# Optimization experiments

Hardware: AMD Instinct MI355X
Metric: run time of the kernel (lower is better)

Reference implementation:

```python
import jax, jax.numpy as jnp
import numpy as np

B, S, D, H = 2, 2048, 1024, 16
HD = D // H  # head_dim = 64
ROPE_BASE = 10000.0
INIT_STD = 0.02


def setup_inputs() -> dict:
    key = jax.random.key(0)
    k1, k2, k3 = jax.random.split(key, 3)
    x = jax.random.normal(k1, (B, S, D), dtype=jnp.float32)
    w_qkv = jax.random.normal(k2, (3 * D, D), dtype=jnp.float32) * INIT_STD
    w_out = jax.random.normal(k3, (D, D), dtype=jnp.float32) * (1.0 / np.sqrt(D))
    b_out = jnp.zeros((D,), dtype=jnp.float32)
    return {"x": x, "w_qkv": w_qkv, "w_out": w_out, "b_out": b_out}


def _rope_cos_sin(s_len, head_dim, dtype):
    theta = 1.0 / ROPE_BASE ** (jnp.arange(0, head_dim, 2, dtype=jnp.float32) / head_dim)
    freqs = jnp.outer(jnp.arange(s_len, dtype=jnp.float32), theta)  # [s, d/2]
    freqs = jnp.concatenate([freqs, freqs], axis=-1)  # [s, d]
    return jnp.cos(freqs).astype(dtype), jnp.sin(freqs).astype(dtype)


def _apply_rope(qk, cos, sin):
    # qk: [b, h, s, d]; rotate-half: (-x2, x1)
    d2 = qk.shape[-1] // 2
    x1, x2 = qk[..., :d2], qk[..., d2:]
    rot = jnp.concatenate([-x2, x1], axis=-1)
    return qk * cos + rot * sin


def reference(x, w_qkv, w_out, b_out):
    b, s, d = x.shape
    qkv = jnp.einsum('bsd,ed->bse', x, w_qkv)  # [b, s, 3D]
    qkv = qkv.reshape(b, s, 3 * H, HD).transpose(0, 2, 1, 3)  # [b, 3h, s, d]
    qk, v = qkv[:, :2 * H], qkv[:, 2 * H:]
    cos, sin = _rope_cos_sin(s, HD, x.dtype)
    qk = _apply_rope(qk, cos, sin)
    q, k = qk[:, :H], qk[:, H:]
    scale = 1.0 / np.sqrt(HD)
    scores = jnp.einsum('bhqd,bhkd->bhqk', q, k) * scale  # [b, h, s, s]
    causal = jnp.tril(jnp.ones((s, s), dtype=bool))
    scores = jnp.where(causal, scores, jnp.finfo(scores.dtype).min)
    attn = jax.nn.softmax(scores, axis=-1)
    o = jnp.einsum('bhqk,bhkd->bhqd', attn, v)  # [b, h, s, d]
    o = o.transpose(0, 2, 1, 3).reshape(b, s, d)
    return jnp.einsum('bsd,ed->bse', o, w_out) + b_out
```

## Files before the change

### kernel.cpp

```cpp
#include <hip/hip_runtime.h>
#include <hip/hip_fp16.h>
#include <math.h>

#define B_  2
#define S_  2048
#define D_  1024
#define H_  16
#define HD_ 64

typedef _Float16  f16;
typedef __attribute__((ext_vector_type(8))) _Float16 f16x8;
typedef __attribute__((ext_vector_type(4))) _Float16 f16x4;
typedef __attribute__((ext_vector_type(4))) float    f32x4;

#define LOG2E 1.4426950408889634f
#define L2_10000_DIV32 0.41524101186092029f
#define PS 72

__device__ __forceinline__ float fin(float v) { return (v == v) ? v : 0.0f; }

__device__ __forceinline__ f16x8 cvt8(const float* p) {
  float4 a = *(const float4*)p;
  float4 b = *(const float4*)(p + 4);
  f16x8 h;
  h[0] = (f16)a.x; h[1] = (f16)a.y; h[2] = (f16)a.z; h[3] = (f16)a.w;
  h[4] = (f16)b.x; h[5] = (f16)b.y; h[6] = (f16)b.z; h[7] = (f16)b.w;
  return h;
}

__device__ __forceinline__ void gload16(const f16* g, f16* l) {
  __builtin_amdgcn_global_load_lds(
      (__attribute__((address_space(1))) void*)(const_cast<f16*>(g)),
      (__attribute__((address_space(3))) void*)l, 16, 0, 0);
}

__global__ void __launch_bounds__(256)
k_cvt3(const float* __restrict__ wq, const float* __restrict__ wo,
       const float* __restrict__ x,
       f16* __restrict__ wqh, f16* __restrict__ woh, f16* __restrict__ xh,
       int doX)
{
  const int NWQ = 3 * D_ * D_ / 4, NWO = D_ * D_ / 4, NX = B_ * S_ * D_ / 4;
  const int n = NWQ + NWO + (doX ? NX : 0);
  for (int i = blockIdx.x * 256 + threadIdx.x; i < n; i += gridDim.x * 256) {
    const float* src; f16* dst; int j;
    if (i < NWQ)            { src = wq; dst = wqh; j = i; }
    else if (i < NWQ + NWO) { src = wo; dst = woh; j = i - NWQ; }
    else                    { src = x;  dst = xh;  j = i - NWQ - NWO; }
    float4 v = ((const float4*)src)[j];
    f16x4 h = {(f16)v.x, (f16)v.y, (f16)v.z, (f16)v.w};
    ((f16x4*)dst)[j] = h;
  }
}

template <bool XF16>
__global__ void __launch_bounds__(256)
k_qkv_rope(const float* __restrict__ xf, const f16* __restrict__ xh,
           const f16* __restrict__ wqh,
           f16* __restrict__ Qb, f16* __restrict__ Kb, f16* __restrict__ Vt)
{
  __shared__ __align__(16) f16 As[128 * 64];
  __shared__ __align__(16) f16 Bs[128 * 64];
  const int t = threadIdx.x;
  const int w = t >> 6;
  const int lane = t & 63;
  const int ll = lane & 15;
  const int quad = lane >> 4;
  const int wm = w >> 1, wn = w & 1;
  const int row0 = blockIdx.y * 128;
  const int col0 = blockIdx.x * 128;

  const f32x4 fz = {0.f, 0.f, 0.f, 0.f};
  f32x4 acc[4][4];
#pragma unroll
  for (int i = 0; i < 4; ++i)
#pragma unroll
    for (int j = 0; j < 4; ++j) acc[i][j] = fz;

  const int ldr = t >> 3;
  const int ldk = (t & 7) * 8;
  const float* gaf = xf  + (size_t)(row0 + ldr) * D_ + ldk;
  const f16*   gah = xh  + (size_t)(row0 + ldr) * D_ + ldk;
  const f16*   gb  = wqh + (size_t)(col0 + ldr) * D_ + ldk;

  for (int kt = 0; kt < D_; kt += 64) {
#pragma unroll
    for (int i = 0; i < 4; ++i) {
      gload16(gb + (size_t)i * 32 * D_ + kt, &Bs[(i * 32 + w * 8) * 64]);
      if (XF16) gload16(gah + (size_t)i * 32 * D_ + kt, &As[(i * 32 + w * 8) * 64]);
    }
    if (!XF16) {
      f16x8 ra[4];
#pragma unroll
      for (int i = 0; i < 4; ++i) ra[i] = cvt8(gaf + (size_t)i * 32 * D_ + kt);
#pragma unroll
      for (int i = 0; i < 4; ++i)
        *(f16x8*)&As[(i * 32 + ldr) * 64 + ldk] = ra[i];
    }
    __syncthreads();
#pragma unroll
    for (int kk = 0; kk < 64; kk += 32) {
      f16x8 a[4], b[4];
#pragma unroll
      for (int mt = 0; mt < 4; ++mt)
        a[mt] = *(const f16x8*)&As[(wm * 64 + mt * 16 + ll) * 64 + kk + quad * 8];
#pragma unroll
      for (int nt = 0; nt < 4; ++nt)
        b[nt] = *(const f16x8*)&Bs[(wn * 64 + nt * 16 + ll) * 64 + kk + quad * 8];
#pragma unroll
      for (int mt = 0; mt < 4; ++mt)
#pragma unroll
        for (int nt = 0; nt < 4; ++nt)
          acc[mt][nt] = __builtin_amdgcn_mfma_f32_16x16x32_f16(
              a[mt], b[nt], acc[mt][nt], 0, 0, 0);
    }
    __syncthreads();
  }

  const int h3 = (col0 >> 6) + wn;
  if (h3 < 32) {
    f16* dst = (h3 < 16) ? Qb : Kb;
    const int h = (h3 < 16) ? h3 : h3 - 16;
    const float th0 = exp2f(-(float)ll * L2_10000_DIV32);
    const float th1 = exp2f(-(float)(16 + ll) * L2_10000_DIV32);
#pragma unroll
    for (int mt = 0; mt < 4; ++mt) {
#pragma unroll
      for (int r = 0; r < 4; ++r) {
        const int row = row0 + wm * 64 + mt * 16 + quad * 4 + r;
        const int b = row >> 11;
        const int p = row & (S_ - 1);
        f16* base = dst + ((size_t)(b * H_ + h) * S_ + p) * HD_;
        const float fp = (float)p;
        float s0, c0, s1, c1;
        sincosf(fp * th0, &s0, &c0);
        sincosf(fp * th1, &s1, &c1);
        {
          float x1 = acc[mt][0][r], x2 = acc[mt][2][r];
          base[ll]      = (f16)fin(x1 * c0 - x2 * s0);
          base[ll + 32] = (f16)fin(x2 * c0 + x1 * s0);
        }
        {
          float x1 = acc[mt][1][r], x2 = acc[mt][3][r];
          base[16 + ll]      = (f16)fin(x1 * c1 - x2 * s1);
          base[16 + ll + 32] = (f16)fin(x2 * c1 + x1 * s1);
        }
      }
    }
  } else {
    const int hv = h3 - 32;
#pragma unroll
    for (int mt = 0; mt < 4; ++mt)
#pragma unroll
      for (int nt = 0; nt < 4; ++nt)
#pragma unroll
        for (int r = 0; r < 4; ++r) {
          const int row = row0 + wm * 64 + mt * 16 + quad * 4 + r;
          const int b = row >> 11;
          const int p = row & (S_ - 1);
          const int dd = nt * 16 + ll;
          Vt[((size_t)(b * H_ + hv) * HD_ + dd) * S_ + p] = (f16)fin(acc[mt][nt][r]);
        }
  }
}

__device__ __forceinline__ void softmax_tile(
    f32x4 sc[4], bool diag, int qloc, int ll, int quad,
    float& mrun, float& lrun, float& alpha, f16* Pt)
{
  float pm = -3.0e4f;
#pragma unroll
  for (int nt = 0; nt < 4; ++nt)
#pragma unroll
    for (int r = 0; r < 4; ++r) {
      float s = sc[nt][r];
      s = (s == s) ? s : -3.0e4f;
      if (diag && (nt * 16 + quad * 4 + r) > qloc) s = -3.0e4f;
      sc[nt][r] = s;
      pm = fmaxf(pm, s);
    }
  pm = fmaxf(pm, __shfl_xor(pm, 16));
  pm = fmaxf(pm, __shfl_xor(pm, 32));
  const float mn = fmaxf(mrun, pm);
  alpha = exp2f(mrun - mn);
  mrun = mn;
  float ps = 0.f;
#pragma unroll
  for (int nt = 0; nt < 4; ++nt) {
    f16x4 pk;
#pragma unroll
    for (int r = 0; r < 4; ++r) {
      float p = exp2f(sc[nt][r] - mn);
      ps += p;
      pk[r] = (f16)p;
    }
    *(f16x4*)&Pt[ll * PS + nt * 16 + quad * 4] = pk;
  }
  ps += __shfl_xor(ps, 16);
  ps += __shfl_xor(ps, 32);
  lrun = lrun * alpha + ps;
}

__device__ __forceinline__ void write_o(
    f32x4 acco[4], float lrun, f16* Pt, int ll, int quad, int w,
    int qt, size_t bh, f16* Ob)
{
  const float inv = 1.0f / fmaxf(lrun, 1e-30f);
#pragma unroll
  for (int dg = 0; dg < 4; ++dg) {
    f16x4 ov;
#pragma unroll
    for (int r = 0; r < 4; ++r) ov[r] = (f16)fin(acco[dg][r] * inv);
    *(f16x4*)&Pt[ll * PS + dg * 16 + quad * 4] = ov;
  }
#pragma unroll
  for (int s2 = 0; s2 < 2; ++s2) {
    f16x8 o = *(const f16x8*)&Pt[ll * PS + (quad + 4 * s2) * 8];
    const size_t row = bh * S_ + qt * 64 + w * 16 + ll;
    *(f16x8*)&Ob[row * HD_ + (quad + 4 * s2) * 8] = o;
  }
}

__global__ void __launch_bounds__(256, 2)
k_attn2(const f16* Qb, const f16* __restrict__ Kb,
        const f16* __restrict__ Vt, f16* Ob)
{
  __shared__ __align__(16) f16 Qs[128 * PS];
  __shared__ __align__(16) f16 Ks[2][64 * PS];
  __shared__ __align__(16) f16 Vs[2][64 * PS];
  __shared__ __align__(16) f16 Ps[4][16 * PS];

  const int t = threadIdx.x;
  const int w = t >> 6;
  const int lane = t & 63;
  const int ll = lane & 15;
  const int quad = lane >> 4;
  const int qtA = blockIdx.x;
  const int qtB = 31 - qtA;
  const int h = blockIdx.y;
  const int b = blockIdx.z;
  const size_t bh = (size_t)b * H_ + h;
  const f16* Qg = Qb + bh * S_ * HD_;
  const f16* Kg = Kb + bh * S_ * HD_;
  const f16* Vg = Vt + bh * HD_ * S_;

  {
    const int r = t >> 1;
    const int c0 = (t & 1) * 32;
    const int grow = (r < 64) ? (qtA * 64 + r) : (qtB * 64 + r - 64);
    const f16 hsc = (f16)(0.125f * LOG2E);
#pragma unroll
    for (int j = 0; j < 4; ++j) {
      f16x8 v = *(const f16x8*)(Qg + (size_t)grow * HD_ + c0 + j * 8);
#pragma unroll
      for (int e = 0; e < 8; ++e) v[e] *= hsc;
      *(f16x8*)&Qs[r * PS + c0 + j * 8] = v;
    }
  }
  {
    const int r = t >> 2;
    const int c = (t & 3) * 16;
    f16x8 a0 = *(const f16x8*)(Kg + (size_t)r * HD_ + c);
    f16x8 a1 = *(const f16x8*)(Kg + (size_t)r * HD_ + c + 8);
    f16x8 b0 = *(const f16x8*)(Vg + (size_t)r * S_ + c);
    f16x8 b1 = *(const f16x8*)(Vg + (size_t)r * S_ + c + 8);
    *(f16x8*)&Ks[0][r * PS + c]     = a0;
    *(f16x8*)&Ks[0][r * PS + c + 8] = a1;
    *(f16x8*)&Vs[0][r * PS + c]     = b0;
    *(f16x8*)&Vs[0][r * PS + c + 8] = b1;
  }
  __syncthreads();

  const f32x4 fz = {0.f, 0.f, 0.f, 0.f};
  f32x4 accoA[4], accoB[4];
#pragma unroll
  for (int i = 0; i < 4; ++i) { accoA[i] = fz; accoB[i] = fz; }
  float mA = -3.0e4f, lA = 0.f, mB = -3.0e4f, lB = 0.f;
  const int qloc = w * 16 + ll;
  f16* Pt = &Ps[w][0];

  for (int kt = 0; kt <= qtB; ++kt) {
    const int cur = kt & 1;
    const bool pre = (kt < qtB);
    const int sr = t >> 2, scc = (t & 3) * 16;
    f16x8 nk0, nk1, nv0, nv1;
    if (pre) {
      const int kn = (kt + 1) * 64;
      nk0 = *(const f16x8*)(Kg + (size_t)(kn + sr) * HD_ + scc);
      nk1 = *(const f16x8*)(Kg + (size_t)(kn + sr) * HD_ + scc + 8);
      nv0 = *(const f16x8*)(Vg + (size_t)sr * S_ + kn + scc);
      nv1 = *(const f16x8*)(Vg + (size_t)sr * S_ + kn + scc + 8);
    }
    const f16* Kc = Ks[cur];
    const f16* Vc = Vs[cur];
    const bool doA = (kt <= qtA);

    f16x8 ak[2][4];
#pragma unroll
    for (int k2 = 0; k2 < 2; ++k2)
#pragma unroll
      for (int nt = 0; nt < 4; ++nt)
        ak[k2][nt] = *(const f16x8*)&Kc[(nt * 16 + ll) * PS + k2 * 32 + quad * 8];

    f32x4 sB[4] = {fz, fz, fz, fz};
#pragma unroll
    for (int k2 = 0; k2 < 2; ++k2) {
      f16x8 bq = *(const f16x8*)&Qs[(64 + w * 16 + ll) * PS + k2 * 32 + quad * 8];
#pragma unroll
      for (int nt = 0; nt < 4; ++nt)
        sB[nt] = __builtin_amdgcn_mfma_f32_16x16x32_f16(ak[k2][nt], bq, sB[nt], 0, 0, 0);
    }
    f32x4 sA[4] = {fz, fz, fz, fz};
    if (doA) {
#pragma unroll
      for (int k2 = 0; k2 < 2; ++k2) {
        f16x8 bq = *(const f16x8*)&Qs[(w * 16 + ll) * PS + k2 * 32 + quad * 8];
#pragma unroll
        for (int nt = 0; nt < 4; ++nt)
          sA[nt] = __builtin_amdgcn_mfma_f32_16x16x32_f16(ak[k2][nt], bq, sA[nt], 0, 0, 0);
      }
    }

    f16x8 av[2][4];
#pragma unroll
    for (int k2 = 0; k2 < 2; ++k2)
#pragma unroll
      for (int dg = 0; dg < 4; ++dg)
        av[k2][dg] = *(const f16x8*)&Vc[(dg * 16 + ll) * PS + k2 * 32 + quad * 8];

    float alpha;
    if (doA) {
      softmax_tile(sA, kt == qtA, qloc, ll, quad, mA, lA, alpha, Pt);
#pragma unroll
      for (int dg = 0; dg < 4; ++dg)
#pragma unroll
        for (int r = 0; r < 4; ++r) accoA[dg][r] *= alpha;
#pragma unroll
      for (int k2 = 0; k2 < 2; ++k2) {
        f16x8 bp = *(const f16x8*)&Pt[ll * PS + k2 * 32 + quad * 8];
#pragma unroll
        for (int dg = 0; dg < 4; ++dg)
          accoA[dg] = __builtin_amdgcn_mfma_f32_16x16x32_f16(av[k2][dg], bp, accoA[dg], 0, 0, 0);
      }
    }
    {
      softmax_tile(sB, kt == qtB, qloc, ll, quad, mB, lB, alpha, Pt);
#pragma unroll
      for (int dg = 0; dg < 4; ++dg)
#pragma unroll
        for (int r = 0; r < 4; ++r) accoB[dg][r] *= alpha;
#pragma unroll
      for (int k2 = 0; k2 < 2; ++k2) {
        f16x8 bp = *(const f16x8*)&Pt[ll * PS + k2 * 32 + quad * 8];
#pragma unroll
        for (int dg = 0; dg < 4; ++dg)
          accoB[dg] = __builtin_amdgcn_mfma_f32_16x16x32_f16(av[k2][dg], bp, accoB[dg], 0, 0, 0);
      }
    }

    if (pre) {
      *(f16x8*)&Ks[1 - cur][sr * PS + scc]     = nk0;
      *(f16x8*)&Ks[1 - cur][sr * PS + scc + 8] = nk1;
      *(f16x8*)&Vs[1 - cur][sr * PS + scc]     = nv0;
      *(f16x8*)&Vs[1 - cur][sr * PS + scc + 8] = nv1;
    }
    __syncthreads();
  }

  write_o(accoA, lA, Pt, ll, quad, w, qtA, bh, Ob);
  write_o(accoB, lB, Pt, ll, quad, w, qtB, bh, Ob);
}

__global__ void __launch_bounds__(256)
k_out_main(const f16* __restrict__ Ob, const f16* __restrict__ Wh,
           const float* __restrict__ bias, float* __restrict__ out)
{
  __shared__ __align__(16) f16 As[128 * 64];
  __shared__ __align__(16) f16 Bs[128 * 64];
  const int t = threadIdx.x;
  const int w = t >> 6;
  const int lane = t & 63;
  const int ll = lane & 15;
  const int quad = lane >> 4;
  const int wm = w >> 1, wn = w & 1;
  const int row0 = blockIdx.y * 128;
  const int col0 = blockIdx.x * 128;
  const int bb = row0 >> 11;
  const int s0 = row0 & (S_ - 1);

  const f32x4 fz = {0.f, 0.f, 0.f, 0.f};
  f32x4 acc[4][4];
#pragma unroll
  for (int i = 0; i < 4; ++i)
#pragma unroll
    for (int j = 0; j < 4; ++j) acc[i][j] = fz;

  const int ldr = t >> 3;
  const int ldk = (t & 7) * 8;
  const f16* gb = Wh + (size_t)(col0 + ldr) * D_ + ldk;

  for (int kt = 0; kt < D_; kt += 64) {
    const int hh = kt >> 6;
    const f16* ga = Ob + (((size_t)(bb * H_ + hh)) * S_ + s0 + ldr) * HD_ + ldk;
#pragma unroll
    for (int i = 0; i < 4; ++i) {
      gload16(ga + (size_t)i * 32 * HD_, &As[(i * 32 + w * 8) * 64]);
      gload16(gb + (size_t)i * 32 * D_ + kt, &Bs[(i * 32 + w * 8) * 64]);
    }
    __syncthreads();
#pragma unroll
    for (int kk = 0; kk < 64; kk += 32) {
      f16x8 a[4], b[4];
#pragma unroll
      for (int mt = 0; mt < 4; ++mt)
        a[mt] = *(const f16x8*)&As[(wm * 64 + mt * 16 + ll) * 64 + kk + quad * 8];
#pragma unroll
      for (int nt = 0; nt < 4; ++nt)
        b[nt] = *(const f16x8*)&Bs[(wn * 64 + nt * 16 + ll) * 64 + kk + quad * 8];
#pragma unroll
      for (int mt = 0; mt < 4; ++mt)
#pragma unroll
        for (int nt = 0; nt < 4; ++nt)
          acc[mt][nt] = __builtin_amdgcn_mfma_f32_16x16x32_f16(
              a[mt], b[nt], acc[mt][nt], 0, 0, 0);
    }
    __syncthreads();
  }

#pragma unroll
  for (int mt = 0; mt < 4; ++mt)
#pragma unroll
    for (int r = 0; r < 4; ++r) {
      const int row = row0 + wm * 64 + mt * 16 + quad * 4 + r;
#pragma unroll
      for (int nt = 0; nt < 4; ++nt) {
        const int col = col0 + wn * 64 + nt * 16 + ll;
        out[(size_t)row * D_ + col] = fin(acc[mt][nt][r] + bias[col]);
      }
    }
}

extern "C" void kernel_launch(void* const* d_in, const int* in_sizes, int n_in,
                              void* d_out, int out_size, void* d_ws, size_t ws_size,
                              hipStream_t stream) {
  const float* x    = (const float*)d_in[0];
  const float* wqkv = (const float*)d_in[1];
  const float* wout = (const float*)d_in[2];
  const float* bout = (const float*)d_in[3];
  float* out = (float*)d_out;

  char* ws = (char*)d_ws;
  f16* wqh = (f16*)(ws);
  f16* Qb  = (f16*)(ws + 6291456);
  f16* Kb  = (f16*)(ws + 14680064);
  f16* Vt  = (f16*)(ws + 23068672);
  f16* woh = (f16*)(ws + 31457280);
  const bool bigws = ws_size >= (size_t)41943040;
  f16* xh  = (f16*)(ws + 33554432);

  k_cvt3<<<2048, 256, 0, stream>>>(wqkv, wout, x, wqh, woh, xh, bigws ? 1 : 0);
  if (bigws)
    k_qkv_rope<true><<<dim3(3 * D_ / 128, (B_ * S_) / 128), 256, 0, stream>>>(
        x, xh, wqh, Qb, Kb, Vt);
  else
    k_qkv_rope<false><<<dim3(3 * D_ / 128, (B_ * S_) / 128), 256, 0, stream>>>(
        x, xh, wqh, Qb, Kb, Vt);
  k_attn2<<<dim3(16, H_, B_), 256, 0, stream>>>(Qb, Kb, Vt, Qb );
  k_out_main<<<dim3(D_ / 128, (B_ * S_) / 128), 256, 0, stream>>>(
      Qb, woh, bout, out);
}
```

Measured before the change: 216.4 us.

## Double-buffer and pad LDS tiles in QKV and output-projection GEMMs

Both GEMM kernels (QKV+RoPE and output projection) drop direct global-to-LDS loads. They now prefetch the next 32-wide K slice into registers while computing on the current slice, using two padded LDS buffers (row stride 36 halves). This aims to overlap global load latency with MFMA work and cut LDS bank conflicts, at the cost of a smaller K step per barrier (32 instead of 64), twice as many iterations and syncs, and extra register pressure.

```diff
diff --git a/kernel.cpp b/kernel.cpp
--- a/kernel.cpp
+++ b/kernel.cpp
@@ -16,6 +16,7 @@
 #define LOG2E 1.4426950408889634f
 #define L2_10000_DIV32 0.41524101186092029f
 #define PS 72
+#define GS 36
 
 __device__ __forceinline__ float fin(float v) { return (v == v) ? v : 0.0f; }
 
@@ -26,12 +27,6 @@
   h[0] = (f16)a.x; h[1] = (f16)a.y; h[2] = (f16)a.z; h[3] = (f16)a.w;
   h[4] = (f16)b.x; h[5] = (f16)b.y; h[6] = (f16)b.z; h[7] = (f16)b.w;
   return h;
-}
-
-__device__ __forceinline__ void gload16(const f16* g, f16* l) {
-  __builtin_amdgcn_global_load_lds(
-      (__attribute__((address_space(1))) void*)(const_cast<f16*>(g)),
-      (__attribute__((address_space(3))) void*)l, 16, 0, 0);
 }
 
 __global__ void __launch_bounds__(256)
@@ -55,12 +50,12 @@
 
 template <bool XF16>
 __global__ void __launch_bounds__(256)
-k_qkv_rope(const float* __restrict__ xf, const f16* __restrict__ xh,
-           const f16* __restrict__ wqh,
-           f16* __restrict__ Qb, f16* __restrict__ Kb, f16* __restrict__ Vt)
+k_qkv2(const float* __restrict__ xf, const f16* __restrict__ xh,
+       const f16* __restrict__ wqh,
+       f16* __restrict__ Qb, f16* __restrict__ Kb, f16* __restrict__ Vt)
 {
-  __shared__ __align__(16) f16 As[128 * 64];
-  __shared__ __align__(16) f16 Bs[128 * 64];
+  __shared__ __align__(16) f16 As[2][128 * GS];
+  __shared__ __align__(16) f16 Bs[2][128 * GS];
   const int t = threadIdx.x;
   const int w = t >> 6;
   const int lane = t & 63;
@@ -70,6 +65,9 @@
   const int row0 = blockIdx.y * 128;
   const int col0 = blockIdx.x * 128;
 
+  const int srow = t >> 2;
+  const int sc   = (t & 3) * 8;
+
   const f32x4 fz = {0.f, 0.f, 0.f, 0.f};
   f32x4 acc[4][4];
 #pragma unroll
@@ -77,42 +75,57 @@
 #pragma unroll
     for (int j = 0; j < 4; ++j) acc[i][j] = fz;
 
-  const int ldr = t >> 3;
-  const int ldk = (t & 7) * 8;
-  const float* gaf = xf  + (size_t)(row0 + ldr) * D_ + ldk;
-  const f16*   gah = xh  + (size_t)(row0 + ldr) * D_ + ldk;
-  const f16*   gb  = wqh + (size_t)(col0 + ldr) * D_ + ldk;
-
-  for (int kt = 0; kt < D_; kt += 64) {
-#pragma unroll
-    for (int i = 0; i < 4; ++i) {
-      gload16(gb + (size_t)i * 32 * D_ + kt, &Bs[(i * 32 + w * 8) * 64]);
-      if (XF16) gload16(gah + (size_t)i * 32 * D_ + kt, &As[(i * 32 + w * 8) * 64]);
-    }
-    if (!XF16) {
-      f16x8 ra[4];
-#pragma unroll
-      for (int i = 0; i < 4; ++i) ra[i] = cvt8(gaf + (size_t)i * 32 * D_ + kt);
-#pragma unroll
-      for (int i = 0; i < 4; ++i)
-        *(f16x8*)&As[(i * 32 + ldr) * 64 + ldk] = ra[i];
-    }
-    __syncthreads();
-#pragma unroll
-    for (int kk = 0; kk < 64; kk += 32) {
-      f16x8 a[4], b[4];
-#pragma unroll
-      for (int mt = 0; mt < 4; ++mt)
-        a[mt] = *(const f16x8*)&As[(wm * 64 + mt * 16 + ll) * 64 + kk + quad * 8];
+  const float* gaf = xf  + (size_t)(row0 + srow) * D_ + sc;
+  const f16*   gah = xh  + (size_t)(row0 + srow) * D_ + sc;
+  const f16*   gb  = wqh + (size_t)(col0 + srow) * D_ + sc;
+
+  f16x8 pa[2], pb[2];
+#pragma unroll
+  for (int i = 0; i < 2; ++i) {
+    pa[i] = XF16 ? *(const f16x8*)(gah + (size_t)i * 64 * D_)
+                 : cvt8(gaf + (size_t)i * 64 * D_);
+    pb[i] = *(const f16x8*)(gb + (size_t)i * 64 * D_);
+  }
+#pragma unroll
+  for (int i = 0; i < 2; ++i) {
+    *(f16x8*)&As[0][(i * 64 + srow) * GS + sc] = pa[i];
+    *(f16x8*)&Bs[0][(i * 64 + srow) * GS + sc] = pb[i];
+  }
+  __syncthreads();
+
+  for (int kt = 0; kt < 32; ++kt) {
+    const int cur = kt & 1;
+    const bool pre = (kt < 31);
+    if (pre) {
+      const int ko = (kt + 1) * 32;
+#pragma unroll
+      for (int i = 0; i < 2; ++i) {
+        pa[i] = XF16 ? *(const f16x8*)(gah + (size_t)i * 64 * D_ + ko)
+                     : cvt8(gaf + (size_t)i * 64 * D_ + ko);
+        pb[i] = *(const f16x8*)(gb + (size_t)i * 64 * D_ + ko);
+      }
+    }
+    const f16* Ac = As[cur];
+    const f16* Bc = Bs[cur];
+    f16x8 a[4], b[4];
+#pragma unroll
+    for (int mt = 0; mt < 4; ++mt)
+      a[mt] = *(const f16x8*)&Ac[(wm * 64 + mt * 16 + ll) * GS + quad * 8];
+#pragma unroll
+    for (int nt = 0; nt < 4; ++nt)
+      b[nt] = *(const f16x8*)&Bc[(wn * 64 + nt * 16 + ll) * GS + quad * 8];
+#pragma unroll
+    for (int mt = 0; mt < 4; ++mt)
 #pragma unroll
       for (int nt = 0; nt < 4; ++nt)
-        b[nt] = *(const f16x8*)&Bs[(wn * 64 + nt * 16 + ll) * 64 + kk + quad * 8];
-#pragma unroll
-      for (int mt = 0; mt < 4; ++mt)
-#pragma unroll
-        for (int nt = 0; nt < 4; ++nt)
-          acc[mt][nt] = __builtin_amdgcn_mfma_f32_16x16x32_f16(
-              a[mt], b[nt], acc[mt][nt], 0, 0, 0);
+        acc[mt][nt] = __builtin_amdgcn_mfma_f32_16x16x32_f16(
+            a[mt], b[nt], acc[mt][nt], 0, 0, 0);
+    if (pre) {
+#pragma unroll
+      for (int i = 0; i < 2; ++i) {
+        *(f16x8*)&As[1 - cur][(i * 64 + srow) * GS + sc] = pa[i];
+        *(f16x8*)&Bs[1 - cur][(i * 64 + srow) * GS + sc] = pb[i];
+      }
     }
     __syncthreads();
   }
@@ -372,11 +385,11 @@
 }
 
 __global__ void __launch_bounds__(256)
-k_out_main(const f16* __restrict__ Ob, const f16* __restrict__ Wh,
-           const float* __restrict__ bias, float* __restrict__ out)
+k_out2(const f16* __restrict__ Ob, const f16* __restrict__ Wh,
+       const float* __restrict__ bias, float* __restrict__ out)
 {
-  __shared__ __align__(16) f16 As[128 * 64];
-  __shared__ __align__(16) f16 Bs[128 * 64];
+  __shared__ __align__(16) f16 As[2][128 * GS];
+  __shared__ __align__(16) f16 Bs[2][128 * GS];
   const int t = threadIdx.x;
   const int w = t >> 6;
   const int lane = t & 63;
@@ -388,6 +401,9 @@
   const int bb = row0 >> 11;
   const int s0 = row0 & (S_ - 1);
 
+  const int srow = t >> 2;
+  const int sc   = (t & 3) * 8;
+
   const f32x4 fz = {0.f, 0.f, 0.f, 0.f};
   f32x4 acc[4][4];
 #pragma unroll
@@ -395,34 +411,56 @@
 #pragma unroll
     for (int j = 0; j < 4; ++j) acc[i][j] = fz;
 
-  const int ldr = t >> 3;
-  const int ldk = (t & 7) * 8;
-  const f16* gb = Wh + (size_t)(col0 + ldr) * D_ + ldk;
-
-  for (int kt = 0; kt < D_; kt += 64) {
-    const int hh = kt >> 6;
-    const f16* ga = Ob + (((size_t)(bb * H_ + hh)) * S_ + s0 + ldr) * HD_ + ldk;
-#pragma unroll
-    for (int i = 0; i < 4; ++i) {
-      gload16(ga + (size_t)i * 32 * HD_, &As[(i * 32 + w * 8) * 64]);
-      gload16(gb + (size_t)i * 32 * D_ + kt, &Bs[(i * 32 + w * 8) * 64]);
-    }
-    __syncthreads();
-#pragma unroll
-    for (int kk = 0; kk < 64; kk += 32) {
-      f16x8 a[4], b[4];
-#pragma unroll
-      for (int mt = 0; mt < 4; ++mt)
-        a[mt] = *(const f16x8*)&As[(wm * 64 + mt * 16 + ll) * 64 + kk + quad * 8];
+  const f16* gb = Wh + (size_t)(col0 + srow) * D_ + sc;
+  const f16* gaBase = Ob + ((size_t)bb * H_ * S_ + s0 + srow) * HD_ + sc;
+
+  f16x8 pa[2], pb[2];
+#pragma unroll
+  for (int i = 0; i < 2; ++i) {
+    pa[i] = *(const f16x8*)(gaBase + (size_t)i * 64 * HD_);
+    pb[i] = *(const f16x8*)(gb + (size_t)i * 64 * D_);
+  }
+#pragma unroll
+  for (int i = 0; i < 2; ++i) {
+    *(f16x8*)&As[0][(i * 64 + srow) * GS + sc] = pa[i];
+    *(f16x8*)&Bs[0][(i * 64 + srow) * GS + sc] = pb[i];
+  }
+  __syncthreads();
+
+  for (int kt = 0; kt < 32; ++kt) {
+    const int cur = kt & 1;
+    const bool pre = (kt < 31);
+    if (pre) {
+      const int kn = kt + 1;
+      const size_t aoff = (size_t)(kn >> 1) * S_ * HD_ + (kn & 1) * 32;
+      const int ko = kn * 32;
+#pragma unroll
+      for (int i = 0; i < 2; ++i) {
+        pa[i] = *(const f16x8*)(gaBase + aoff + (size_t)i * 64 * HD_);
+        pb[i] = *(const f16x8*)(gb + (size_t)i * 64 * D_ + ko);
+      }
+    }
+    const f16* Ac = As[cur];
+    const f16* Bc = Bs[cur];
+    f16x8 a[4], b[4];
+#pragma unroll
+    for (int mt = 0; mt < 4; ++mt)
+      a[mt] = *(const f16x8*)&Ac[(wm * 64 + mt * 16 + ll) * GS + quad * 8];
+#pragma unroll
+    for (int nt = 0; nt < 4; ++nt)
+      b[nt] = *(const f16x8*)&Bc[(wn * 64 + nt * 16 + ll) * GS + quad * 8];
+#pragma unroll
+    for (int mt = 0; mt < 4; ++mt)
 #pragma unroll
       for (int nt = 0; nt < 4; ++nt)
-        b[nt] = *(const f16x8*)&Bs[(wn * 64 + nt * 16 + ll) * 64 + kk + quad * 8];
-#pragma unroll
-      for (int mt = 0; mt < 4; ++mt)
-#pragma unroll
-        for (int nt = 0; nt < 4; ++nt)
-          acc[mt][nt] = __builtin_amdgcn_mfma_f32_16x16x32_f16(
-              a[mt], b[nt], acc[mt][nt], 0, 0, 0);
+        acc[mt][nt] = __builtin_amdgcn_mfma_f32_16x16x32_f16(
+            a[mt], b[nt], acc[mt][nt], 0, 0, 0);
+    if (pre) {
+#pragma unroll
+      for (int i = 0; i < 2; ++i) {
+        *(f16x8*)&As[1 - cur][(i * 64 + srow) * GS + sc] = pa[i];
+        *(f16x8*)&Bs[1 - cur][(i * 64 + srow) * GS + sc] = pb[i];
+      }
     }
     __syncthreads();
   }
@@ -460,12 +498,12 @@
 
   k_cvt3<<<2048, 256, 0, stream>>>(wqkv, wout, x, wqh, woh, xh, bigws ? 1 : 0);
   if (bigws)
-    k_qkv_rope<true><<<dim3(3 * D_ / 128, (B_ * S_) / 128), 256, 0, stream>>>(
+    k_qkv2<true><<<dim3(3 * D_ / 128, (B_ * S_) / 128), 256, 0, stream>>>(
         x, xh, wqh, Qb, Kb, Vt);
   else
-    k_qkv_rope<false><<<dim3(3 * D_ / 128, (B_ * S_) / 128), 256, 0, stream>>>(
+    k_qkv2<false><<<dim3(3 * D_ / 128, (B_ * S_) / 128), 256, 0, stream>>>(
         x, xh, wqh, Qb, Kb, Vt);
   k_attn2<<<dim3(16, H_, B_), 256, 0, stream>>>(Qb, Kb, Vt, Qb );
-  k_out_main<<<dim3(D_ / 128, (B_ * S_) / 128), 256, 0, stream>>>(
+  k_out2<<<dim3(D_ / 128, (B_ * S_) / 128), 256, 0, stream>>>(
       Qb, woh, bout, out);
 }
```

After: 282.3 us. +30.4%, slower.

## Replace direct-to-LDS loads with padded register-staged tiles in projection GEMMs

Applied to the files above, without the earlier changes.

Both projection GEMMs stop using global_load_lds and instead load tiles into registers, then write them to LDS with a padded row stride of 72 halfs to avoid bank conflicts on the MFMA fragment reads. The register loads are issued before the barrier, so they overlap with the previous iteration's MFMAs, and the trailing barrier is removed. The output projection also drops to 64-row tiles, doubling the grid to improve occupancy and wave balance on the small GEMM. The cost is higher register pressure and LDS use, plus an extra register round trip per tile.

```diff
diff --git a/kernel.cpp b/kernel.cpp
--- a/kernel.cpp
+++ b/kernel.cpp
@@ -26,12 +26,6 @@
   h[0] = (f16)a.x; h[1] = (f16)a.y; h[2] = (f16)a.z; h[3] = (f16)a.w;
   h[4] = (f16)b.x; h[5] = (f16)b.y; h[6] = (f16)b.z; h[7] = (f16)b.w;
   return h;
-}
-
-__device__ __forceinline__ void gload16(const f16* g, f16* l) {
-  __builtin_amdgcn_global_load_lds(
-      (__attribute__((address_space(1))) void*)(const_cast<f16*>(g)),
-      (__attribute__((address_space(3))) void*)l, 16, 0, 0);
 }
 
 __global__ void __launch_bounds__(256)
@@ -55,12 +49,12 @@
 
 template <bool XF16>
 __global__ void __launch_bounds__(256)
-k_qkv_rope(const float* __restrict__ xf, const f16* __restrict__ xh,
-           const f16* __restrict__ wqh,
-           f16* __restrict__ Qb, f16* __restrict__ Kb, f16* __restrict__ Vt)
-{
-  __shared__ __align__(16) f16 As[128 * 64];
-  __shared__ __align__(16) f16 Bs[128 * 64];
+k_qkv3(const float* __restrict__ xf, const f16* __restrict__ xh,
+       const f16* __restrict__ wqh,
+       f16* __restrict__ Qb, f16* __restrict__ Kb, f16* __restrict__ Vt)
+{
+  __shared__ __align__(16) f16 As[128 * PS];
+  __shared__ __align__(16) f16 Bs[128 * PS];
   const int t = threadIdx.x;
   const int w = t >> 6;
   const int lane = t & 63;
@@ -84,18 +78,18 @@
   const f16*   gb  = wqh + (size_t)(col0 + ldr) * D_ + ldk;
 
   for (int kt = 0; kt < D_; kt += 64) {
+    f16x8 ra[4], rb[4];
 #pragma unroll
     for (int i = 0; i < 4; ++i) {
-      gload16(gb + (size_t)i * 32 * D_ + kt, &Bs[(i * 32 + w * 8) * 64]);
-      if (XF16) gload16(gah + (size_t)i * 32 * D_ + kt, &As[(i * 32 + w * 8) * 64]);
-    }
-    if (!XF16) {
-      f16x8 ra[4];
-#pragma unroll
-      for (int i = 0; i < 4; ++i) ra[i] = cvt8(gaf + (size_t)i * 32 * D_ + kt);
-#pragma unroll
-      for (int i = 0; i < 4; ++i)
-        *(f16x8*)&As[(i * 32 + ldr) * 64 + ldk] = ra[i];
+      ra[i] = XF16 ? *(const f16x8*)(gah + (size_t)i * 32 * D_ + kt)
+                   : cvt8(gaf + (size_t)i * 32 * D_ + kt);
+      rb[i] = *(const f16x8*)(gb + (size_t)i * 32 * D_ + kt);
+    }
+    __syncthreads();
+#pragma unroll
+    for (int i = 0; i < 4; ++i) {
+      *(f16x8*)&As[(i * 32 + ldr) * PS + ldk] = ra[i];
+      *(f16x8*)&Bs[(i * 32 + ldr) * PS + ldk] = rb[i];
     }
     __syncthreads();
 #pragma unroll
@@ -103,10 +97,10 @@
       f16x8 a[4], b[4];
 #pragma unroll
       for (int mt = 0; mt < 4; ++mt)
-        a[mt] = *(const f16x8*)&As[(wm * 64 + mt * 16 + ll) * 64 + kk + quad * 8];
+        a[mt] = *(const f16x8*)&As[(wm * 64 + mt * 16 + ll) * PS + kk + quad * 8];
 #pragma unroll
       for (int nt = 0; nt < 4; ++nt)
-        b[nt] = *(const f16x8*)&Bs[(wn * 64 + nt * 16 + ll) * 64 + kk + quad * 8];
+        b[nt] = *(const f16x8*)&Bs[(wn * 64 + nt * 16 + ll) * PS + kk + quad * 8];
 #pragma unroll
       for (int mt = 0; mt < 4; ++mt)
 #pragma unroll
@@ -114,7 +108,6 @@
           acc[mt][nt] = __builtin_amdgcn_mfma_f32_16x16x32_f16(
               a[mt], b[nt], acc[mt][nt], 0, 0, 0);
     }
-    __syncthreads();
   }
 
   const int h3 = (col0 >> 6) + wn;
@@ -372,26 +365,26 @@
 }
 
 __global__ void __launch_bounds__(256)
-k_out_main(const f16* __restrict__ Ob, const f16* __restrict__ Wh,
-           const float* __restrict__ bias, float* __restrict__ out)
-{
-  __shared__ __align__(16) f16 As[128 * 64];
-  __shared__ __align__(16) f16 Bs[128 * 64];
+k_out3(const f16* __restrict__ Ob, const f16* __restrict__ Wh,
+       const float* __restrict__ bias, float* __restrict__ out)
+{
+  __shared__ __align__(16) f16 As[64 * PS];
+  __shared__ __align__(16) f16 Bs[128 * PS];
   const int t = threadIdx.x;
   const int w = t >> 6;
   const int lane = t & 63;
   const int ll = lane & 15;
   const int quad = lane >> 4;
   const int wm = w >> 1, wn = w & 1;
-  const int row0 = blockIdx.y * 128;
+  const int row0 = blockIdx.y * 64;
   const int col0 = blockIdx.x * 128;
   const int bb = row0 >> 11;
   const int s0 = row0 & (S_ - 1);
 
   const f32x4 fz = {0.f, 0.f, 0.f, 0.f};
-  f32x4 acc[4][4];
-#pragma unroll
-  for (int i = 0; i < 4; ++i)
+  f32x4 acc[2][4];
+#pragma unroll
+  for (int i = 0; i < 2; ++i)
 #pragma unroll
     for (int j = 0; j < 4; ++j) acc[i][j] = fz;
 
@@ -399,39 +392,46 @@
   const int ldk = (t & 7) * 8;
   const f16* gb = Wh + (size_t)(col0 + ldr) * D_ + ldk;
 
-  for (int kt = 0; kt < D_; kt += 64) {
-    const int hh = kt >> 6;
-    const f16* ga = Ob + (((size_t)(bb * H_ + hh)) * S_ + s0 + ldr) * HD_ + ldk;
-#pragma unroll
-    for (int i = 0; i < 4; ++i) {
-      gload16(ga + (size_t)i * 32 * HD_, &As[(i * 32 + w * 8) * 64]);
-      gload16(gb + (size_t)i * 32 * D_ + kt, &Bs[(i * 32 + w * 8) * 64]);
-    }
+  for (int kt = 0; kt < 16; ++kt) {
+    const f16* ga = Ob + (((size_t)(bb * H_ + kt)) * S_ + s0 + ldr) * HD_ + ldk;
+    f16x8 ra[2], rb[4];
+#pragma unroll
+    for (int i = 0; i < 2; ++i)
+      ra[i] = *(const f16x8*)(ga + (size_t)i * 32 * HD_);
+#pragma unroll
+    for (int i = 0; i < 4; ++i)
+      rb[i] = *(const f16x8*)(gb + (size_t)i * 32 * D_ + kt * 64);
     __syncthreads();
 #pragma unroll
+    for (int i = 0; i < 2; ++i)
+      *(f16x8*)&As[(i * 32 + ldr) * PS + ldk] = ra[i];
+#pragma unroll
+    for (int i = 0; i < 4; ++i)
+      *(f16x8*)&Bs[(i * 32 + ldr) * PS + ldk] = rb[i];
+    __syncthreads();
+#pragma unroll
     for (int kk = 0; kk < 64; kk += 32) {
-      f16x8 a[4], b[4];
-#pragma unroll
-      for (int mt = 0; mt < 4; ++mt)
-        a[mt] = *(const f16x8*)&As[(wm * 64 + mt * 16 + ll) * 64 + kk + quad * 8];
+      f16x8 a[2], b[4];
+#pragma unroll
+      for (int mt = 0; mt < 2; ++mt)
+        a[mt] = *(const f16x8*)&As[(wm * 32 + mt * 16 + ll) * PS + kk + quad * 8];
 #pragma unroll
       for (int nt = 0; nt < 4; ++nt)
-        b[nt] = *(const f16x8*)&Bs[(wn * 64 + nt * 16 + ll) * 64 + kk + quad * 8];
-#pragma unroll
-      for (int mt = 0; mt < 4; ++mt)
+        b[nt] = *(const f16x8*)&Bs[(wn * 64 + nt * 16 + ll) * PS + kk + quad * 8];
+#pragma unroll
+      for (int mt = 0; mt < 2; ++mt)
 #pragma unroll
         for (int nt = 0; nt < 4; ++nt)
           acc[mt][nt] = __builtin_amdgcn_mfma_f32_16x16x32_f16(
               a[mt], b[nt], acc[mt][nt], 0, 0, 0);
     }
-    __syncthreads();
-  }
-
-#pragma unroll
-  for (int mt = 0; mt < 4; ++mt)
+  }
+
+#pragma unroll
+  for (int mt = 0; mt < 2; ++mt)
 #pragma unroll
     for (int r = 0; r < 4; ++r) {
-      const int row = row0 + wm * 64 + mt * 16 + quad * 4 + r;
+      const int row = row0 + wm * 32 + mt * 16 + quad * 4 + r;
 #pragma unroll
       for (int nt = 0; nt < 4; ++nt) {
         const int col = col0 + wn * 64 + nt * 16 + ll;
@@ -460,12 +460,12 @@
 
   k_cvt3<<<2048, 256, 0, stream>>>(wqkv, wout, x, wqh, woh, xh, bigws ? 1 : 0);
   if (bigws)
-    k_qkv_rope<true><<<dim3(3 * D_ / 128, (B_ * S_) / 128), 256, 0, stream>>>(
+    k_qkv3<true><<<dim3(3 * D_ / 128, (B_ * S_) / 128), 256, 0, stream>>>(
         x, xh, wqh, Qb, Kb, Vt);
   else
-    k_qkv_rope<false><<<dim3(3 * D_ / 128, (B_ * S_) / 128), 256, 0, stream>>>(
+    k_qkv3<false><<<dim3(3 * D_ / 128, (B_ * S_) / 128), 256, 0, stream>>>(
         x, xh, wqh, Qb, Kb, Vt);
   k_attn2<<<dim3(16, H_, B_), 256, 0, stream>>>(Qb, Kb, Vt, Qb );
-  k_out_main<<<dim3(D_ / 128, (B_ * S_) / 128), 256, 0, stream>>>(
+  k_out3<<<dim3(D_ / 128, (B_ * S_) / 64), 256, 0, stream>>>(
       Qb, woh, bout, out);
 }
```

Result: faster. 195.4 us (-9.7%).
